# Optimization experiments

Measured on AMD Instinct MI355X. Metric: run time of the kernel, lower is better.

## Reference

```python
import jax, jax.numpy as jnp
import numpy as np

GROUPS = 32
NUM_HEADS = 8
EPS = 1e-5


def setup_inputs() -> dict:
    key = jax.random.key(0)
    ks = jax.random.split(key, 8)
    b, c, h, w = 2, 256, 64, 64
    x = jax.random.normal(ks[0], (b, c, h, w), dtype=jnp.float32)
    gn_w = jnp.ones((c,), dtype=jnp.float32)
    gn_b = jnp.zeros((c,), dtype=jnp.float32)
    qkv_w = jax.random.normal(ks[1], (3 * c, c), dtype=jnp.float32) * 0.02  # 1x1 conv
    qkv_b = jnp.zeros((3 * c,), dtype=jnp.float32)
    proj_w = jax.random.normal(ks[2], (c, c), dtype=jnp.float32) * 0.02  # 1x1 conv
    proj_b = jnp.zeros((c,), dtype=jnp.float32)
    return {"x": x, "gn_w": gn_w, "gn_b": gn_b, "qkv_w": qkv_w,
            "qkv_b": qkv_b, "proj_w": proj_w, "proj_b": proj_b}


def _group_norm(x, w, b):
    bsz, c, h, wd = x.shape
    xg = x.reshape(bsz, GROUPS, c // GROUPS, h * wd)
    mean = jnp.mean(xg, axis=(2, 3), keepdims=True)
    var = jnp.mean(jnp.square(xg - mean), axis=(2, 3), keepdims=True)
    xn = ((xg - mean) * jax.lax.rsqrt(var + EPS)).reshape(bsz, c, h, wd)
    return xn * w[None, :, None, None] + b[None, :, None, None]


def reference(x, gn_w, gn_b, qkv_w, qkv_b, proj_w, proj_b):
    b, c, h, w = x.shape
    hd = c // NUM_HEADS
    s = h * w
    xn = _group_norm(x, gn_w, gn_b)
    # 1x1 conv == channel matmul
    qkv = jnp.einsum('oc,bcs->bos', qkv_w, xn.reshape(b, c, s)) + qkv_b[None, :, None]
    qkv = qkv.reshape(b, 3, NUM_HEADS, hd, s)
    q, k, v = qkv[:, 0], qkv[:, 1], qkv[:, 2]  # (b, nh, hd, s)
    scale = 1.0 / jnp.sqrt(jnp.asarray(hd, dtype=x.dtype))
    scores = jnp.einsum('bhds,bhdt->bhst', q, k) * scale  # (b, nh, s, s)
    attn = jax.nn.softmax(scores, axis=-1)
    out = jnp.einsum('bhst,bhdt->bhds', attn, v)  # (b, nh, hd, s)
    out = out.reshape(b, c, h, w)
    out = jnp.einsum('oc,bcs->bos', proj_w, out.reshape(b, c, s)).reshape(b, c, h, w)
    out = out + proj_b[None, :, None, None]
    return out + x
```

## Files before the change

kernel.cpp:

```cpp
#include <hip/hip_runtime.h>
#include <hip/hip_bf16.h>

#define B_ 2
#define C_ 256
#define S_ 4096
#define NH 8
#define HD 32
#define EPSV 1e-5f
#define QSC2 0.25503487942324256f

typedef __bf16 bf16_t;
typedef bf16_t bf16x8 __attribute__((ext_vector_type(8)));
typedef float f32x4 __attribute__((ext_vector_type(4)));
typedef float f32x16 __attribute__((ext_vector_type(16)));
typedef int i32x2 __attribute__((ext_vector_type(2)));
typedef __hip_bfloat16 hbf;

__device__ inline unsigned cvtpk_bf16(float a, float b) {
  unsigned r;
  asm("v_cvt_pk_bf16_f32 %0, %1, %2" : "=v"(r) : "v"(a), "v"(b));
  return r;
}

#if __has_builtin(__builtin_amdgcn_exp2f)
#define EXP2R(x) __builtin_amdgcn_exp2f(x)
#else
#define EXP2R(x) exp2f(x)
#endif

__global__ __launch_bounds__(256) void f2bf_kernel(const float* __restrict__ src, hbf* __restrict__ dst, int n) {
  int i = blockIdx.x * 256 + threadIdx.x;
  if (i < n) dst[i] = __float2bfloat16(src[i]);
}

__global__ __launch_bounds__(1024) void gn_kernel(const float* __restrict__ x, const float* __restrict__ gw,
                                                  const float* __restrict__ gb, hbf* __restrict__ xn_t) {
  int b = blockIdx.x >> 5, g = blockIdx.x & 31;
  const float* xp = x + ((size_t)b * C_ + g * 8) * S_;
  float sum = 0.f, sumsq = 0.f;
  const float4* xp4 = (const float4*)xp;
  for (int i = threadIdx.x; i < 8 * S_ / 4; i += 1024) {
    float4 v = xp4[i];
    sum += v.x + v.y + v.z + v.w;
    sumsq += v.x * v.x + v.y * v.y + v.z * v.z + v.w * v.w;
  }
#pragma unroll
  for (int off = 32; off > 0; off >>= 1) {
    sum += __shfl_down(sum, off);
    sumsq += __shfl_down(sumsq, off);
  }
  __shared__ float red[2][16];
  int wid = threadIdx.x >> 6;
  if ((threadIdx.x & 63) == 0) { red[0][wid] = sum; red[1][wid] = sumsq; }
  __syncthreads();
  sum = 0.f; sumsq = 0.f;
#pragma unroll
  for (int k = 0; k < 16; k++) { sum += red[0][k]; sumsq += red[1][k]; }
  const float inv_n = 1.f / (8 * S_);
  float mean = sum * inv_n;
  float rstd = rsqrtf(fmaxf(sumsq * inv_n - mean * mean, 0.f) + EPSV);
  float scv[8], shv[8];
#pragma unroll
  for (int c = 0; c < 8; c++) {
    scv[c] = gw[g * 8 + c] * rstd;
    shv[c] = gb[g * 8 + c] - mean * scv[c];
  }
  hbf* outp = xn_t + (size_t)b * S_ * C_ + g * 8;
  for (int s = threadIdx.x; s < S_; s += 1024) {
    alignas(16) hbf tmp[8];
#pragma unroll
    for (int c = 0; c < 8; c++)
      tmp[c] = __float2bfloat16(xp[(size_t)c * S_ + s] * scv[c] + shv[c]);
    *(uint4*)&outp[(size_t)s * C_] = *(uint4*)tmp;
  }
}

__global__ __launch_bounds__(256) void qkv_gemm(const hbf* __restrict__ xn_t, const hbf* __restrict__ wb,
                                                const float* __restrict__ bias,
                                                hbf* __restrict__ qbuf, hbf* __restrict__ kg,
                                                hbf* __restrict__ vg) {
  int bt = blockIdx.z;
  int m0 = blockIdx.x * 64;
  int n0 = blockIdx.y * 64;
  const hbf* A = xn_t + (size_t)bt * S_ * C_;
  __shared__ hbf a_lds[64][72];
  __shared__ hbf b_lds[64][72];
  int tid = threadIdx.x, lane = tid & 63, wid = tid >> 6;
  int wm = (wid >> 1) * 32, wn = (wid & 1) * 32;
  f32x4 acc[2][2] = {};
  for (int k0 = 0; k0 < C_; k0 += 64) {
    __syncthreads();
    int r = tid >> 3, kk = (tid & 7) * 8;
#pragma unroll
    for (int p = 0; p < 2; p++) {
      *(bf16x8*)&a_lds[r + p * 32][kk] = *(const bf16x8*)&A[(size_t)(m0 + r + p * 32) * C_ + k0 + kk];
      *(bf16x8*)&b_lds[r + p * 32][kk] = *(const bf16x8*)&wb[(size_t)(n0 + r + p * 32) * C_ + k0 + kk];
    }
    __syncthreads();
#pragma unroll
    for (int kk2 = 0; kk2 < 64; kk2 += 32) {
      bf16x8 af[2], bfr[2];
#pragma unroll
      for (int mi = 0; mi < 2; mi++)
        af[mi] = *(const bf16x8*)&a_lds[wm + mi * 16 + (lane & 15)][kk2 + (lane >> 4) * 8];
#pragma unroll
      for (int ni = 0; ni < 2; ni++)
        bfr[ni] = *(const bf16x8*)&b_lds[wn + ni * 16 + (lane & 15)][kk2 + (lane >> 4) * 8];
#pragma unroll
      for (int mi = 0; mi < 2; mi++)
#pragma unroll
        for (int ni = 0; ni < 2; ni++)
          acc[mi][ni] = __builtin_amdgcn_mfma_f32_16x16x32_bf16(af[mi], bfr[ni], acc[mi][ni], 0, 0, 0);
    }
  }
#pragma unroll
  for (int mi = 0; mi < 2; mi++)
#pragma unroll
    for (int ni = 0; ni < 2; ni++) {
      int o = n0 + wn + ni * 16 + (lane & 15);
      int s = m0 + wm + mi * 16 + (lane >> 4) * 4;
      float bs = bias[o];
      f32x4 v = acc[mi][ni];
      if (o < 256) {
#pragma unroll
        for (int rr = 0; rr < 4; rr++)
          qbuf[((size_t)bt * S_ + s + rr) * C_ + o] = __float2bfloat16((v[rr] + bs) * QSC2);
      } else if (o < 512) {
        int hh = (o - 256) >> 5, dd = (o - 256) & 31;
        size_t base = (((size_t)(bt * NH + hh) * (S_ >> 5) + (s >> 5)) * 2 + (dd >> 4)) * 512 + (dd & 15);
#pragma unroll
        for (int rr = 0; rr < 4; rr++)
          kg[base + (size_t)((s & 31) + rr) * 16] = __float2bfloat16(v[rr] + bs);
      } else {
        int hh = (o - 512) >> 5, dd = (o - 512) & 31;
        alignas(8) hbf tmp[4];
#pragma unroll
        for (int rr = 0; rr < 4; rr++) tmp[rr] = __float2bfloat16(v[rr] + bs);
        *(uint2*)&vg[(((size_t)(bt * NH + hh) * (S_ >> 4) + (s >> 4)) * 32 + dd) * 16 + (s & 15)] = *(uint2*)tmp;
      }
    }
}

__device__ inline void softmax_pv(f32x16 sc, bf16x8 va0, bf16x8 va1,
                                  f32x16& o_acc, float& l_run) {
#pragma unroll
  for (int i = 0; i < 16; i++) sc[i] = EXP2R(sc[i]);
  {
    float s0a = sc[0] + sc[1], s1a = sc[2] + sc[3], s2a = sc[4] + sc[5], s3a = sc[6] + sc[7];
    float s4a = sc[8] + sc[9], s5a = sc[10] + sc[11], s6a = sc[12] + sc[13], s7a = sc[14] + sc[15];
    s0a += s1a; s2a += s3a; s4a += s5a; s6a += s7a;
    s0a += s2a; s4a += s6a;
    l_run += s0a + s4a;
  }
#pragma unroll
  for (int kb = 0; kb < 2; kb++) {
    unsigned a0 = cvtpk_bf16(sc[kb * 8 + 0], sc[kb * 8 + 1]);
    unsigned b0 = cvtpk_bf16(sc[kb * 8 + 2], sc[kb * 8 + 3]);
    unsigned a1 = cvtpk_bf16(sc[kb * 8 + 4], sc[kb * 8 + 5]);
    unsigned b1 = cvtpk_bf16(sc[kb * 8 + 6], sc[kb * 8 + 7]);
    i32x2 ra = __builtin_amdgcn_permlane32_swap((int)a0, (int)a1, false, false);
    i32x2 rb = __builtin_amdgcn_permlane32_swap((int)b0, (int)b1, false, false);
    union { unsigned u[4]; bf16x8 v; } pf;
    pf.u[0] = (unsigned)ra[0]; pf.u[1] = (unsigned)rb[0];
    pf.u[2] = (unsigned)ra[1]; pf.u[3] = (unsigned)rb[1];
    o_acc = __builtin_amdgcn_mfma_f32_32x32x16_bf16(kb ? va1 : va0, pf.v, o_acc, 0, 0, 0);
  }
}

__global__ __launch_bounds__(512, 4) void attn_kernel(const hbf* __restrict__ qbuf, const hbf* __restrict__ kg,
                                                      const hbf* __restrict__ vg, hbf* __restrict__ attn_t) {
  int bid = blockIdx.x;
  int xcd = bid & 7, idx = bid >> 3;
  int combo = (xcd << 1) | (idx >> 6);
  int bt = combo >> 3, h = combo & 7;
  int s0 = (idx & 63) << 6;
  int tid = threadIdx.x, lane = tid & 63, w = tid >> 6;
  int wq = w & 1, wt = w >> 1;
  int l31 = lane & 31, hi = lane >> 5;
  const int loff = (l31 << 4) + (hi << 3);
  int qrow = s0 + wq * 32 + l31;
  bf16x8 qf0 = *(const bf16x8*)&qbuf[((size_t)bt * S_ + qrow) * C_ + h * HD + hi * 8];
  bf16x8 qf1 = *(const bf16x8*)&qbuf[((size_t)bt * S_ + qrow) * C_ + h * HD + 16 + hi * 8];
  f32x16 o_acc = {0.f,0.f,0.f,0.f,0.f,0.f,0.f,0.f,0.f,0.f,0.f,0.f,0.f,0.f,0.f,0.f};
  const f32x16 z16 = o_acc;
  float l_run = 0.f;
  const int tq0 = wt << 10;
  const hbf* kq = kg + ((size_t)(bt * NH + h) * (S_ >> 5) + (tq0 >> 5)) * 1024;
  const hbf* vq = vg + ((size_t)(bt * NH + h) * (S_ >> 4) + (tq0 >> 4)) * 512;
  bf16x8 ka0 = *(const bf16x8*)(kq + loff);
  bf16x8 ka1 = *(const bf16x8*)(kq + loff + 512);
  bf16x8 va0 = *(const bf16x8*)(vq + loff);
  bf16x8 va1 = *(const bf16x8*)(vq + loff + 512);
  f32x16 sc = __builtin_amdgcn_mfma_f32_32x32x16_bf16(ka0, qf0, z16, 0, 0, 0);
  sc = __builtin_amdgcn_mfma_f32_32x32x16_bf16(ka1, qf1, sc, 0, 0, 0);
  ka0 = *(const bf16x8*)(kq + 1024 + loff);
  ka1 = *(const bf16x8*)(kq + 1024 + loff + 512);
  kq += 2048;
  vq += 1024;
  for (int it = 1; it < 32; ++it) {
    bf16x8 kan0 = *(const bf16x8*)(kq + loff);
    bf16x8 kan1 = *(const bf16x8*)(kq + loff + 512);
    bf16x8 van0 = *(const bf16x8*)(vq + loff);
    bf16x8 van1 = *(const bf16x8*)(vq + loff + 512);
    f32x16 scn = __builtin_amdgcn_mfma_f32_32x32x16_bf16(ka0, qf0, z16, 0, 0, 0);
    scn = __builtin_amdgcn_mfma_f32_32x32x16_bf16(ka1, qf1, scn, 0, 0, 0);
    softmax_pv(sc, va0, va1, o_acc, l_run);
    sc = scn;
    ka0 = kan0; ka1 = kan1; va0 = van0; va1 = van1;
    kq += 1024; vq += 1024;
  }
  softmax_pv(sc, va0, va1, o_acc, l_run);
  __shared__ f32x16 ored[6 * 64];
  __shared__ float lred[8 * 64];
  __syncthreads();
  lred[(w << 6) + lane] = l_run;
  if (wt > 0) ored[((w - 2) << 6) + lane] = o_acc;
  __syncthreads();
  if (wt == 0) {
    float l_tot = 0.f;
#pragma unroll
    for (int k = 0; k < 4; k++) {
      int wp = wq + 2 * k;
      l_tot += lred[(wp << 6) + l31] + lred[(wp << 6) + 32 + l31];
    }
    f32x16 o = o_acc;
#pragma unroll
    for (int k = 0; k < 3; k++) {
      f32x16 t2 = ored[((wq + 2 * k) << 6) + lane];
#pragma unroll
      for (int i = 0; i < 16; i++) o[i] += t2[i];
    }
    float inv_l = 1.0f / l_tot;
#pragma unroll
    for (int c2 = 0; c2 < 4; c2++) {
      alignas(8) hbf tmp[4];
#pragma unroll
      for (int r = 0; r < 4; r++) tmp[r] = __float2bfloat16(o[c2 * 4 + r] * inv_l);
      *(uint2*)&attn_t[((size_t)bt * S_ + qrow) * C_ + h * HD + c2 * 8 + hi * 4] = *(uint2*)tmp;
    }
  }
}

__global__ __launch_bounds__(256) void proj_gemm(const hbf* __restrict__ attn_t, const hbf* __restrict__ wb,
                                                 const float* __restrict__ bias, const float* __restrict__ x,
                                                 float* __restrict__ out) {
  int bt = blockIdx.z;
  int m0 = blockIdx.x * 64;
  int n0 = blockIdx.y * 64;
  const hbf* A = attn_t + (size_t)bt * S_ * C_;
  __shared__ hbf a_lds[64][72];
  __shared__ hbf b_lds[64][72];
  int tid = threadIdx.x, lane = tid & 63, wid = tid >> 6;
  int wm = (wid >> 1) * 32, wn = (wid & 1) * 32;
  f32x4 acc[2][2] = {};
  for (int k0 = 0; k0 < C_; k0 += 64) {
    __syncthreads();
    int r = tid >> 3, kk = (tid & 7) * 8;
#pragma unroll
    for (int p = 0; p < 2; p++) {
      *(bf16x8*)&a_lds[r + p * 32][kk] = *(const bf16x8*)&A[(size_t)(m0 + r + p * 32) * C_ + k0 + kk];
      *(bf16x8*)&b_lds[r + p * 32][kk] = *(const bf16x8*)&wb[(size_t)(n0 + r + p * 32) * C_ + k0 + kk];
    }
    __syncthreads();
#pragma unroll
    for (int kk2 = 0; kk2 < 64; kk2 += 32) {
      bf16x8 af[2], bfr[2];
#pragma unroll
      for (int mi = 0; mi < 2; mi++)
        af[mi] = *(const bf16x8*)&a_lds[wm + mi * 16 + (lane & 15)][kk2 + (lane >> 4) * 8];
#pragma unroll
      for (int ni = 0; ni < 2; ni++)
        bfr[ni] = *(const bf16x8*)&b_lds[wn + ni * 16 + (lane & 15)][kk2 + (lane >> 4) * 8];
#pragma unroll
      for (int mi = 0; mi < 2; mi++)
#pragma unroll
        for (int ni = 0; ni < 2; ni++)
          acc[mi][ni] = __builtin_amdgcn_mfma_f32_16x16x32_bf16(af[mi], bfr[ni], acc[mi][ni], 0, 0, 0);
    }
  }
#pragma unroll
  for (int mi = 0; mi < 2; mi++)
#pragma unroll
    for (int ni = 0; ni < 2; ni++) {
      int o = n0 + wn + ni * 16 + (lane & 15);
      int s = m0 + wm + mi * 16 + (lane >> 4) * 4;
      size_t base = ((size_t)bt * C_ + o) * S_ + s;
      float pb = bias[o];
      float4 xr = *(const float4*)&x[base];
      float4 res;
      res.x = acc[mi][ni][0] + pb + xr.x;
      res.y = acc[mi][ni][1] + pb + xr.y;
      res.z = acc[mi][ni][2] + pb + xr.z;
      res.w = acc[mi][ni][3] + pb + xr.w;
      *(float4*)&out[base] = res;
    }
}

extern "C" void kernel_launch(void* const* d_in, const int* in_sizes, int n_in,
                              void* d_out, int out_size, void* d_ws, size_t ws_size,
                              hipStream_t stream) {
  const float* x = (const float*)d_in[0];
  const float* gn_w = (const float*)d_in[1];
  const float* gn_b = (const float*)d_in[2];
  const float* qkv_w = (const float*)d_in[3];
  const float* qkv_b = (const float*)d_in[4];
  const float* proj_w = (const float*)d_in[5];
  const float* proj_b = (const float*)d_in[6];
  float* out = (float*)d_out;

  hbf* qkv_w_bf = (hbf*)d_ws;
  hbf* proj_w_bf = qkv_w_bf + 768 * 256;
  hbf* xn_t = proj_w_bf + 256 * 256;
  hbf* qbuf = xn_t + (size_t)B_ * S_ * C_;
  hbf* kg = qbuf + (size_t)B_ * S_ * C_;
  hbf* vg = kg + (size_t)B_ * S_ * C_;
  hbf* attn_t = vg + (size_t)B_ * S_ * C_;

  dim3 blk(256);
  f2bf_kernel<<<(768 * 256 + 255) / 256, blk, 0, stream>>>(qkv_w, qkv_w_bf, 768 * 256);
  f2bf_kernel<<<(256 * 256 + 255) / 256, blk, 0, stream>>>(proj_w, proj_w_bf, 256 * 256);
  gn_kernel<<<64, dim3(1024), 0, stream>>>(x, gn_w, gn_b, xn_t);
  qkv_gemm<<<dim3(64, 12, 2), blk, 0, stream>>>(xn_t, qkv_w_bf, qkv_b, qbuf, kg, vg);
  attn_kernel<<<dim3(1024), dim3(512), 0, stream>>>(qbuf, kg, vg, attn_t);
  proj_gemm<<<dim3(64, 4, 2), blk, 0, stream>>>(attn_t, proj_w_bf, proj_b, x, out);
}
```

Before: 89.71 us.

## Prepack GN output and QKV weights into MFMA fragment layout, drop LDS in QKV GEMM

GroupNorm now writes its bf16 output directly in a 32x16 MFMA-fragment-tiled layout, and a new kernel repacks the QKV weights the same way. The QKV GEMM then loads operands straight from global memory into registers with no shared-memory staging or barriers, using 32x32x16 MFMA on 128x128 tiles with 512 threads. This removes LDS traffic and synchronisation in the projection GEMM. In exchange, operand reuse now relies on cache rather than LDS, and the epilogue stores become scalar scattered bf16 writes.

```diff
diff --git a/kernel.cpp b/kernel.cpp
--- a/kernel.cpp
+++ b/kernel.cpp
@@ -33,8 +33,18 @@
   if (i < n) dst[i] = __float2bfloat16(src[i]);
 }
 
+__global__ __launch_bounds__(256) void wfrag_kernel(const float* __restrict__ src, hbf* __restrict__ dst, int nchunks) {
+  int i = blockIdx.x * 256 + threadIdx.x;
+  if (i >= nchunks) return;
+  int o = i >> 5, c8 = (i & 31) * 8;
+  alignas(16) hbf tmp[8];
+#pragma unroll
+  for (int j = 0; j < 8; j++) tmp[j] = __float2bfloat16(src[(size_t)o * C_ + c8 + j]);
+  *(uint4*)&dst[(((size_t)(o >> 5) * 16) + (c8 >> 4)) * 512 + (o & 31) * 16 + (c8 & 15)] = *(uint4*)tmp;
+}
+
 __global__ __launch_bounds__(1024) void gn_kernel(const float* __restrict__ x, const float* __restrict__ gw,
-                                                  const float* __restrict__ gb, hbf* __restrict__ xn_t) {
+                                                  const float* __restrict__ gb, hbf* __restrict__ xn) {
   int b = blockIdx.x >> 5, g = blockIdx.x & 31;
   const float* xp = x + ((size_t)b * C_ + g * 8) * S_;
   float sum = 0.f, sumsq = 0.f;
@@ -65,80 +75,73 @@
     scv[c] = gw[g * 8 + c] * rstd;
     shv[c] = gb[g * 8 + c] - mean * scv[c];
   }
-  hbf* outp = xn_t + (size_t)b * S_ * C_ + g * 8;
   for (int s = threadIdx.x; s < S_; s += 1024) {
     alignas(16) hbf tmp[8];
 #pragma unroll
     for (int c = 0; c < 8; c++)
       tmp[c] = __float2bfloat16(xp[(size_t)c * S_ + s] * scv[c] + shv[c]);
-    *(uint4*)&outp[(size_t)s * C_] = *(uint4*)tmp;
-  }
-}
-
-__global__ __launch_bounds__(256) void qkv_gemm(const hbf* __restrict__ xn_t, const hbf* __restrict__ wb,
-                                                const float* __restrict__ bias,
-                                                hbf* __restrict__ qbuf, hbf* __restrict__ kg,
-                                                hbf* __restrict__ vg) {
+    *(uint4*)&xn[(((size_t)b * (S_ >> 5) + (s >> 5)) * 16 + (g >> 1)) * 512 + (s & 31) * 16 + (g & 1) * 8] =
+        *(uint4*)tmp;
+  }
+}
+
+__global__ __launch_bounds__(512, 4) void qkv_gemm(const hbf* __restrict__ xn, const hbf* __restrict__ wf,
+                                                   const float* __restrict__ bias,
+                                                   hbf* __restrict__ qbuf, hbf* __restrict__ kg,
+                                                   hbf* __restrict__ vg) {
   int bt = blockIdx.z;
-  int m0 = blockIdx.x * 64;
-  int n0 = blockIdx.y * 64;
-  const hbf* A = xn_t + (size_t)bt * S_ * C_;
-  __shared__ hbf a_lds[64][72];
-  __shared__ hbf b_lds[64][72];
-  int tid = threadIdx.x, lane = tid & 63, wid = tid >> 6;
-  int wm = (wid >> 1) * 32, wn = (wid & 1) * 32;
-  f32x4 acc[2][2] = {};
-  for (int k0 = 0; k0 < C_; k0 += 64) {
-    __syncthreads();
-    int r = tid >> 3, kk = (tid & 7) * 8;
-#pragma unroll
-    for (int p = 0; p < 2; p++) {
-      *(bf16x8*)&a_lds[r + p * 32][kk] = *(const bf16x8*)&A[(size_t)(m0 + r + p * 32) * C_ + k0 + kk];
-      *(bf16x8*)&b_lds[r + p * 32][kk] = *(const bf16x8*)&wb[(size_t)(n0 + r + p * 32) * C_ + k0 + kk];
-    }
-    __syncthreads();
-#pragma unroll
-    for (int kk2 = 0; kk2 < 64; kk2 += 32) {
-      bf16x8 af[2], bfr[2];
-#pragma unroll
-      for (int mi = 0; mi < 2; mi++)
-        af[mi] = *(const bf16x8*)&a_lds[wm + mi * 16 + (lane & 15)][kk2 + (lane >> 4) * 8];
-#pragma unroll
-      for (int ni = 0; ni < 2; ni++)
-        bfr[ni] = *(const bf16x8*)&b_lds[wn + ni * 16 + (lane & 15)][kk2 + (lane >> 4) * 8];
-#pragma unroll
-      for (int mi = 0; mi < 2; mi++)
-#pragma unroll
-        for (int ni = 0; ni < 2; ni++)
-          acc[mi][ni] = __builtin_amdgcn_mfma_f32_16x16x32_bf16(af[mi], bfr[ni], acc[mi][ni], 0, 0, 0);
-    }
-  }
-#pragma unroll
-  for (int mi = 0; mi < 2; mi++)
-#pragma unroll
-    for (int ni = 0; ni < 2; ni++) {
-      int o = n0 + wn + ni * 16 + (lane & 15);
-      int s = m0 + wm + mi * 16 + (lane >> 4) * 4;
-      float bs = bias[o];
-      f32x4 v = acc[mi][ni];
-      if (o < 256) {
-#pragma unroll
-        for (int rr = 0; rr < 4; rr++)
-          qbuf[((size_t)bt * S_ + s + rr) * C_ + o] = __float2bfloat16((v[rr] + bs) * QSC2);
-      } else if (o < 512) {
-        int hh = (o - 256) >> 5, dd = (o - 256) & 31;
-        size_t base = (((size_t)(bt * NH + hh) * (S_ >> 5) + (s >> 5)) * 2 + (dd >> 4)) * 512 + (dd & 15);
-#pragma unroll
-        for (int rr = 0; rr < 4; rr++)
-          kg[base + (size_t)((s & 31) + rr) * 16] = __float2bfloat16(v[rr] + bs);
-      } else {
-        int hh = (o - 512) >> 5, dd = (o - 512) & 31;
-        alignas(8) hbf tmp[4];
-#pragma unroll
-        for (int rr = 0; rr < 4; rr++) tmp[rr] = __float2bfloat16(v[rr] + bs);
-        *(uint2*)&vg[(((size_t)(bt * NH + hh) * (S_ >> 4) + (s >> 4)) * 32 + dd) * 16 + (s & 15)] = *(uint2*)tmp;
+  int m0 = blockIdx.x * 128;
+  int n0 = blockIdx.y * 128;
+  int tid = threadIdx.x, lane = tid & 63, w = tid >> 6;
+  int wq = w & 3, wo = w >> 2;
+  int l31 = lane & 31, hi = lane >> 5;
+  const int loff = l31 * 16 + hi * 8;
+  const hbf* ap = xn + ((size_t)bt * (S_ >> 5) + (m0 >> 5) + wq) * 8192;
+  int oc0 = n0 + wo * 64;
+  const hbf* bp0 = wf + (size_t)(oc0 >> 5) * 8192;
+  const hbf* bp1 = bp0 + 8192;
+  f32x16 acc0 = {0.f,0.f,0.f,0.f,0.f,0.f,0.f,0.f,0.f,0.f,0.f,0.f,0.f,0.f,0.f,0.f};
+  f32x16 acc1 = acc0;
+#pragma unroll 4
+  for (int ks = 0; ks < 16; ++ks) {
+    bf16x8 af = *(const bf16x8*)(ap + ks * 512 + loff);
+    bf16x8 b0 = *(const bf16x8*)(bp0 + ks * 512 + loff);
+    bf16x8 b1 = *(const bf16x8*)(bp1 + ks * 512 + loff);
+    acc0 = __builtin_amdgcn_mfma_f32_32x32x16_bf16(af, b0, acc0, 0, 0, 0);
+    acc1 = __builtin_amdgcn_mfma_f32_32x32x16_bf16(af, b1, acc1, 0, 0, 0);
+  }
+  int s_base = m0 + wq * 32;
+#pragma unroll
+  for (int ct = 0; ct < 2; ++ct) {
+    f32x16 a = ct ? acc1 : acc0;
+    int oc = oc0 + ct * 32;
+    int o = oc + l31;
+    float bs = bias[o];
+    if (oc < 256) {
+#pragma unroll
+      for (int r = 0; r < 16; r++) {
+        int s = s_base + (r & 3) + 8 * (r >> 2) + 4 * hi;
+        qbuf[((size_t)bt * S_ + s) * C_ + o] = __float2bfloat16((a[r] + bs) * QSC2);
       }
-    }
+    } else if (oc < 512) {
+      int hh = (oc - 256) >> 5;
+      const size_t khead = (size_t)(bt * NH + hh) * (S_ >> 5);
+#pragma unroll
+      for (int r = 0; r < 16; r++) {
+        int s = s_base + (r & 3) + 8 * (r >> 2) + 4 * hi;
+        kg[(khead + (s >> 5)) * 1024 + (l31 >> 4) * 512 + (s & 31) * 16 + (l31 & 15)] =
+            __float2bfloat16(a[r] + bs);
+      }
+    } else {
+      int hh = (oc - 512) >> 5;
+      const size_t vhead = (size_t)(bt * NH + hh) * (S_ >> 4);
+#pragma unroll
+      for (int r = 0; r < 16; r++) {
+        int s = s_base + (r & 3) + 8 * (r >> 2) + 4 * hi;
+        vg[(vhead + (s >> 4)) * 512 + l31 * 16 + (s & 15)] = __float2bfloat16(a[r] + bs);
+      }
+    }
+  }
 }
 
 __device__ inline void softmax_pv(f32x16 sc, bf16x8 va0, bf16x8 va1,
@@ -308,19 +311,19 @@
   const float* proj_b = (const float*)d_in[6];
   float* out = (float*)d_out;
 
-  hbf* qkv_w_bf = (hbf*)d_ws;
-  hbf* proj_w_bf = qkv_w_bf + 768 * 256;
-  hbf* xn_t = proj_w_bf + 256 * 256;
-  hbf* qbuf = xn_t + (size_t)B_ * S_ * C_;
+  hbf* qkv_wf = (hbf*)d_ws;
+  hbf* proj_w_bf = qkv_wf + 768 * 256;
+  hbf* xn = proj_w_bf + 256 * 256;
+  hbf* qbuf = xn + (size_t)B_ * S_ * C_;
   hbf* kg = qbuf + (size_t)B_ * S_ * C_;
   hbf* vg = kg + (size_t)B_ * S_ * C_;
   hbf* attn_t = vg + (size_t)B_ * S_ * C_;
 
   dim3 blk(256);
-  f2bf_kernel<<<(768 * 256 + 255) / 256, blk, 0, stream>>>(qkv_w, qkv_w_bf, 768 * 256);
+  wfrag_kernel<<<(768 * 32 + 255) / 256, blk, 0, stream>>>(qkv_w, qkv_wf, 768 * 32);
   f2bf_kernel<<<(256 * 256 + 255) / 256, blk, 0, stream>>>(proj_w, proj_w_bf, 256 * 256);
-  gn_kernel<<<64, dim3(1024), 0, stream>>>(x, gn_w, gn_b, xn_t);
-  qkv_gemm<<<dim3(64, 12, 2), blk, 0, stream>>>(xn_t, qkv_w_bf, qkv_b, qbuf, kg, vg);
+  gn_kernel<<<64, dim3(1024), 0, stream>>>(x, gn_w, gn_b, xn);
+  qkv_gemm<<<dim3(32, 6, 2), dim3(512), 0, stream>>>(xn, qkv_wf, qkv_b, qbuf, kg, vg);
   attn_kernel<<<dim3(1024), dim3(512), 0, stream>>>(qbuf, kg, vg, attn_t);
   proj_gemm<<<dim3(64, 4, 2), blk, 0, stream>>>(attn_t, proj_w_bf, proj_b, x, out);
 }
```

After: 85.43 us. 4.8% less time.
